# Performance work log

Measured on AMD Instinct MI355X. Metric: run time of the kernel, lower is better.

## Reference

```python
import jax, jax.numpy as jnp
import numpy as np

N_NODES = 100000
N_EDGES = 1600000
D_IN = 256
D_OUT = 64
BN_EPS = 1e-5


def setup_inputs() -> dict:
    key = jax.random.key(0)
    ks = jax.random.split(key, 8)
    x = jax.random.normal(ks[0], (N_NODES, D_IN), dtype=jnp.float32)
    edge_index = jax.random.randint(ks[1], (2, N_EDGES), 0, N_NODES, dtype=jnp.int32)
    W = jax.random.normal(ks[2], (D_OUT, D_IN), dtype=jnp.float32) / np.sqrt(D_IN).astype(np.float32)
    bias = 0.01 * jax.random.normal(ks[3], (D_OUT,), dtype=jnp.float32)
    gamma = 1.0 + 0.1 * jax.random.normal(ks[4], (D_OUT,), dtype=jnp.float32)
    beta = 0.1 * jax.random.normal(ks[5], (D_OUT,), dtype=jnp.float32)
    running_mean = 0.1 * jax.random.normal(ks[6], (D_OUT,), dtype=jnp.float32)
    running_var = jax.random.uniform(ks[7], (D_OUT,), dtype=jnp.float32, minval=0.5, maxval=1.5)
    return {"x": x, "edge_index": edge_index, "W": W, "bias": bias,
            "gamma": gamma, "beta": beta,
            "running_mean": running_mean, "running_var": running_var}


def reference(x, edge_index, W, bias, gamma, beta, running_mean, running_var):
    # GCNConv (PyG semantics): transform -> symmetric-normalized scatter-add with
    # self-loops (edge_weight = ones, self-loop weight = 1), then +bias.
    n = x.shape[0]
    loop = jnp.arange(n, dtype=edge_index.dtype)
    row = jnp.concatenate([edge_index[0], loop])  # source nodes
    col = jnp.concatenate([edge_index[1], loop])  # target nodes
    w = jnp.ones(row.shape[0], dtype=x.dtype)
    deg = jax.ops.segment_sum(w, col, num_segments=n)          # [N]
    dinv = jnp.where(deg > 0, jax.lax.rsqrt(deg), 0.0)          # D^{-1/2}
    norm = dinv[row] * w * dinv[col]                            # [E+N]
    xw = x @ W.T                                                # [N, D_OUT]
    agg = jax.ops.segment_sum(norm[:, None] * xw[row], col, num_segments=n)
    out = agg + bias
    # BatchNorm1d in eval mode (running stats); dropout inactive in eval.
    out = (out - running_mean) * jax.lax.rsqrt(running_var + BN_EPS) * gamma + beta
    return jax.nn.relu(out)
```

## Files before the change

### kernel.cpp

```cpp
#include <hip/hip_runtime.h>
#include <hip/hip_bf16.h>

#define D_IN 256
#define D_OUT 64
#define BN_EPS 1e-5f

#define BINSHIFT 8
#define BINCAP 4608
#define PCHUNK 8192

typedef __attribute__((ext_vector_type(4))) float floatx4;
typedef __attribute__((ext_vector_type(8))) __bf16 bf16x8;
typedef __attribute__((ext_vector_type(4))) unsigned uintx4;

__global__ __launch_bounds__(256) void k_prep(
        const float* __restrict__ W, __bf16* __restrict__ whi, __bf16* __restrict__ wlo,
        const float* __restrict__ bias, const float* __restrict__ gamma,
        const float* __restrict__ beta, const float* __restrict__ rmean,
        const float* __restrict__ rvar,
        float* __restrict__ bnsc, float* __restrict__ bnsh,
        int* __restrict__ bincur, int nbins) {
    int b = blockIdx.x, t = threadIdx.x;
    if (b < 2) {
        int i = b * 256 + t;
        if (i < nbins) bincur[i] = 0;
        if (b == 1 && t < D_OUT) {
            float sc = rsqrtf(rvar[t] + BN_EPS) * gamma[t];
            bnsc[t] = sc;
            bnsh[t] = (bias[t] - rmean[t]) * sc + beta[t];
        }
        return;
    }
    int tid = (b - 2) * 256 + t;
    int lane = tid & 63, c = (tid >> 6) & 7, tt = tid >> 9;
    int row = tt * 16 + (lane & 15);
    int k0 = c * 32 + (lane >> 4) * 8;
    size_t dst = (size_t)tid * 8;
    #pragma unroll
    for (int j = 0; j < 8; ++j) {
        float w = W[(size_t)row * D_IN + k0 + j];
        __bf16 h = (__bf16)w;
        whi[dst + j] = h;
        wlo[dst + j] = (__bf16)(w - (float)h);
    }
}

__global__ __launch_bounds__(256) void k_part(
        const int* __restrict__ ei, int* __restrict__ bincur,
        unsigned* __restrict__ pairs, int E, int nbins) {
    __shared__ int hist[512];
    __shared__ int base[512];
    int t = threadIdx.x;
    int e0 = blockIdx.x * PCHUNK;

    for (int j = t; j < nbins; j += 256) hist[j] = 0;
    __syncthreads();

    int cols[PCHUNK / 256];
    int ranks[PCHUNK / 256];
    #pragma unroll
    for (int i = 0; i < PCHUNK / 256; ++i) {
        int e = e0 + i * 256 + t;
        if (e < E) {
            int c = ei[E + e];
            cols[i] = c;
            ranks[i] = atomicAdd(&hist[c >> BINSHIFT], 1);
        }
    }
    __syncthreads();
    for (int j = t; j < nbins; j += 256)
        base[j] = atomicAdd(&bincur[j], hist[j]);
    __syncthreads();
    #pragma unroll
    for (int i = 0; i < PCHUNK / 256; ++i) {
        int e = e0 + i * 256 + t;
        if (e < E) {
            int c = cols[i];
            int bin = c >> BINSHIFT;
            int pos = base[bin] + ranks[i];
            if (pos >= BINCAP) pos = BINCAP - 1;
            pairs[(size_t)bin * BINCAP + pos] =
                ((unsigned)ei[e] << 8) | (unsigned)(c & 255);
        }
    }
}

__global__ __launch_bounds__(256) void k_binscan(
        const int* __restrict__ bincur, int* __restrict__ binoff,
        int* __restrict__ off, int nbins, int N) {
    __shared__ int sc[256];
    int t = threadIdx.x;
    int i0 = 2 * t, i1 = 2 * t + 1;
    int v0 = (i0 < nbins) ? bincur[i0] : 0;
    int v1 = (i1 < nbins) ? bincur[i1] : 0;
    int s = v0 + v1;
    sc[t] = s;
    __syncthreads();
    for (int o = 1; o < 256; o <<= 1) {
        int v = (t >= o) ? sc[t - o] : 0;
        __syncthreads();
        sc[t] += v;
        __syncthreads();
    }
    int excl = sc[t] - s;
    if (i0 < nbins) binoff[i0] = excl;
    if (i1 < nbins) binoff[i1] = excl + v0;
    if (t == 255) off[N] = sc[255];
}

__global__ __launch_bounds__(256) void k_fill3(
        const unsigned* __restrict__ pairs, const int* __restrict__ bincur,
        const int* __restrict__ binoff, int* __restrict__ off,
        float* __restrict__ dinv, int* __restrict__ srcs, int n) {
    __shared__ int hist[256];
    __shared__ int sc[256];
    __shared__ int curs[256];
    int bin = blockIdx.x, t = threadIdx.x;
    hist[t] = 0;
    __syncthreads();
    int cnt = bincur[bin];
    const unsigned* bp = pairs + (size_t)bin * BINCAP;
    for (int p = t; p < cnt; p += 256)
        atomicAdd(&hist[bp[p] & 255u], 1);
    __syncthreads();
    int own = hist[t];
    sc[t] = own;
    __syncthreads();
    for (int o = 1; o < 256; o <<= 1) {
        int v = (t >= o) ? sc[t - o] : 0;
        __syncthreads();
        sc[t] += v;
        __syncthreads();
    }
    int base = binoff[bin] + sc[t] - own;
    int node = (bin << BINSHIFT) + t;
    curs[t] = base;
    if (node < n) {
        off[node] = base;
        dinv[node] = rsqrtf((float)(own + 1));
    }
    __syncthreads();
    for (int p = t; p < cnt; p += 256) {
        unsigned v = bp[p];
        int pos = atomicAdd(&curs[v & 255u], 1);
        srcs[pos] = (int)(v >> 8);
    }
}

__global__ __launch_bounds__(256) void k_gemm(
        const float* __restrict__ x, const __bf16* __restrict__ whi,
        const __bf16* __restrict__ wlo, const float* __restrict__ dinv,
        __bf16* __restrict__ yb, int n) {
    int wave = threadIdx.x >> 6;
    int lane = threadIdx.x & 63;
    int m0 = blockIdx.x * 64 + wave * 16;
    if (m0 >= n) return;
    int q = lane >> 4, cl = lane & 15;
    int arow = m0 + cl; if (arow >= n) arow = n - 1;
    const float* ap = x + (size_t)arow * D_IN + q * 8;

    floatx4 acc[4] = {{0.f,0.f,0.f,0.f},{0.f,0.f,0.f,0.f},
                      {0.f,0.f,0.f,0.f},{0.f,0.f,0.f,0.f}};

    #pragma unroll
    for (int c = 0; c < 8; ++c) {
        floatx4 a0 = *(const floatx4*)(ap + c * 32);
        floatx4 a1 = *(const floatx4*)(ap + c * 32 + 4);
        bf16x8 ahi, alo;
        #pragma unroll
        for (int j = 0; j < 4; ++j) {
            __bf16 h0 = (__bf16)a0[j];
            __bf16 h1 = (__bf16)a1[j];
            ahi[j] = h0;     alo[j] = (__bf16)(a0[j] - (float)h0);
            ahi[4 + j] = h1; alo[4 + j] = (__bf16)(a1[j] - (float)h1);
        }
        #pragma unroll
        for (int t = 0; t < 4; ++t) {
            size_t fo = ((size_t)(t * 8 + c) * 64 + lane) * 8;
            bf16x8 bh = *(const bf16x8*)(whi + fo);
            bf16x8 bl = *(const bf16x8*)(wlo + fo);
            acc[t] = __builtin_amdgcn_mfma_f32_16x16x32_bf16(ahi, bh, acc[t], 0, 0, 0);
            acc[t] = __builtin_amdgcn_mfma_f32_16x16x32_bf16(alo, bh, acc[t], 0, 0, 0);
            acc[t] = __builtin_amdgcn_mfma_f32_16x16x32_bf16(ahi, bl, acc[t], 0, 0, 0);
        }
    }

    int nb = m0 + q * 4;
    float dv[4];
    #pragma unroll
    for (int r = 0; r < 4; ++r) dv[r] = (nb + r < n) ? dinv[nb + r] : 0.f;
    #pragma unroll
    for (int t = 0; t < 4; ++t) {
        #pragma unroll
        for (int r = 0; r < 4; ++r) {
            int node = nb + r;
            if (node < n)
                yb[(size_t)node * D_OUT + t * 16 + cl] = (__bf16)(dv[r] * acc[t][r]);
        }
    }
}

__device__ __forceinline__ void acc_row4(uintx4 v, float (&a)[8]) {
    #pragma unroll
    for (int k = 0; k < 4; ++k) {
        a[2 * k]     += __uint_as_float(v[k] << 16);
        a[2 * k + 1] += __uint_as_float(v[k] & 0xffff0000u);
    }
}

__global__ __launch_bounds__(256) void k_aggregate(
        const int* __restrict__ off, const int* __restrict__ srcs,
        const unsigned* __restrict__ ybf, const float* __restrict__ dinv,
        const float* __restrict__ bnsc, const float* __restrict__ bnsh,
        float* __restrict__ out, int n) {
    int node = blockIdx.x * 4 + (threadIdx.x >> 6);
    if (node >= n) return;
    int lane = threadIdx.x & 63;
    int g = lane >> 3, sl = lane & 7;
    int s = off[node], e2 = off[node + 1];

    float a[8] = {0.f, 0.f, 0.f, 0.f, 0.f, 0.f, 0.f, 0.f};
    float dv = 0.f;
    floatx4 bs0, bs1, bh0, bh1;
    if (g == 0) {
        dv = dinv[node];
        bs0 = *(const floatx4*)(bnsc + sl * 8);
        bs1 = *(const floatx4*)(bnsc + sl * 8 + 4);
        bh0 = *(const floatx4*)(bnsh + sl * 8);
        bh1 = *(const floatx4*)(bnsh + sl * 8 + 4);
        uintx4 v = *(const uintx4*)(ybf + (size_t)node * 32 + sl * 4);
        acc_row4(v, a);
    }

    int e = s + g;
    for (; e + 24 < e2; e += 32) {
        int r0 = srcs[e], r1 = srcs[e + 8], r2 = srcs[e + 16], r3 = srcs[e + 24];
        uintx4 v0 = *(const uintx4*)(ybf + (size_t)r0 * 32 + sl * 4);
        uintx4 v1 = *(const uintx4*)(ybf + (size_t)r1 * 32 + sl * 4);
        uintx4 v2 = *(const uintx4*)(ybf + (size_t)r2 * 32 + sl * 4);
        uintx4 v3 = *(const uintx4*)(ybf + (size_t)r3 * 32 + sl * 4);
        acc_row4(v0, a);
        acc_row4(v1, a);
        acc_row4(v2, a);
        acc_row4(v3, a);
    }
    for (; e + 8 < e2; e += 16) {
        int r0 = srcs[e], r1 = srcs[e + 8];
        uintx4 v0 = *(const uintx4*)(ybf + (size_t)r0 * 32 + sl * 4);
        uintx4 v1 = *(const uintx4*)(ybf + (size_t)r1 * 32 + sl * 4);
        acc_row4(v0, a);
        acc_row4(v1, a);
    }
    for (; e < e2; e += 8) {
        uintx4 v = *(const uintx4*)(ybf + (size_t)srcs[e] * 32 + sl * 4);
        acc_row4(v, a);
    }

    #pragma unroll
    for (int k = 0; k < 8; ++k) {
        a[k] += __shfl_xor(a[k], 8);
        a[k] += __shfl_xor(a[k], 16);
        a[k] += __shfl_xor(a[k], 32);
    }

    if (g == 0) {
        float o[8];
        #pragma unroll
        for (int k = 0; k < 4; ++k) {
            o[k]     = fmaf(dv * a[k],     bs0[k], bh0[k]);
            o[4 + k] = fmaf(dv * a[4 + k], bs1[k], bh1[k]);
        }
        floatx4 w0 = { fmaxf(o[0], 0.f), fmaxf(o[1], 0.f),
                       fmaxf(o[2], 0.f), fmaxf(o[3], 0.f) };
        floatx4 w1 = { fmaxf(o[4], 0.f), fmaxf(o[5], 0.f),
                       fmaxf(o[6], 0.f), fmaxf(o[7], 0.f) };
        *(floatx4*)(out + (size_t)node * D_OUT + sl * 8) = w0;
        *(floatx4*)(out + (size_t)node * D_OUT + sl * 8 + 4) = w1;
    }
}

static inline char* align_up(char* p, size_t a) {
    return (char*)(((uintptr_t)p + a - 1) & ~(uintptr_t)(a - 1));
}

extern "C" void kernel_launch(void* const* d_in, const int* in_sizes, int n_in,
                              void* d_out, int out_size, void* d_ws, size_t ws_size,
                              hipStream_t stream) {
    const float* x     = (const float*)d_in[0];
    const int*   ei    = (const int*)d_in[1];
    const float* W     = (const float*)d_in[2];
    const float* bias  = (const float*)d_in[3];
    const float* gamma = (const float*)d_in[4];
    const float* beta  = (const float*)d_in[5];
    const float* rmean = (const float*)d_in[6];
    const float* rvar  = (const float*)d_in[7];
    float* out = (float*)d_out;

    int N = in_sizes[0] / D_IN;
    int E = in_sizes[1] / 2;
    int nbins = (N + (1 << BINSHIFT) - 1) >> BINSHIFT;

    char* p = (char*)d_ws;
    int*      bincur = (int*)p;         p += 512 * 4;
    int*      binoff = (int*)p;         p += 512 * 4;
    int*      off    = (int*)p;         p += (size_t)(N + 1) * 4; p = align_up(p, 256);
    float*    dinv   = (float*)p;       p += (size_t)N * 4;       p = align_up(p, 256);
    float*    bnsc   = (float*)p;       p += D_OUT * 4;
    float*    bnsh   = (float*)p;       p += D_OUT * 4;           p = align_up(p, 256);
    __bf16*   whi    = (__bf16*)p;      p += (size_t)D_OUT * D_IN * 2; p = align_up(p, 256);
    __bf16*   wlo    = (__bf16*)p;      p += (size_t)D_OUT * D_IN * 2; p = align_up(p, 256);
    __bf16*   yb     = (__bf16*)p;      p += (size_t)N * D_OUT * 2;    p = align_up(p, 256);
    int*      srcs   = (int*)p;         p += (size_t)E * 4;       p = align_up(p, 256);
    unsigned* pairs  = (unsigned*)p;

    k_prep<<<10, 256, 0, stream>>>(W, whi, wlo, bias, gamma, beta, rmean, rvar,
                                   bnsc, bnsh, bincur, nbins);
    k_part<<<(E + PCHUNK - 1) / PCHUNK, 256, 0, stream>>>(ei, bincur, pairs, E, nbins);
    k_binscan<<<1, 256, 0, stream>>>(bincur, binoff, off, nbins, N);
    k_fill3<<<nbins, 256, 0, stream>>>(pairs, bincur, binoff, off, dinv, srcs, N);
    k_gemm<<<(N + 63) / 64, 256, 0, stream>>>(x, whi, wlo, dinv, yb, N);
    k_aggregate<<<(N + 3) / 4, 256, 0, stream>>>(off, srcs, (const unsigned*)yb,
                                                 dinv, bnsc, bnsh, out, N);
}
```

Measured before the change: 289.2 us.

## Fuse partition, bin scan and fill into one cooperative kernel with grid sync

Merges the three CSR-build kernels (edge partition into bins, bin prefix scan, per-bin fill) into a single cooperative launch with nbins blocks separated by grid-wide syncs. Each block now partitions about E/nbins edges instead of a fixed 8192-edge chunk. Edges beyond the first 16 per thread fall back to global atomics on the bin counters. This removes two kernel launches and their gaps, but the partition phase now runs on 391 blocks instead of 196, and the fallback path makes more global atomics.

```diff
diff --git a/kernel.cpp b/kernel.cpp
--- a/kernel.cpp
+++ b/kernel.cpp
@@ -1,5 +1,8 @@
 #include <hip/hip_runtime.h>
 #include <hip/hip_bf16.h>
+#include <hip/hip_cooperative_groups.h>
+
+namespace cg = cooperative_groups;
 
 #define D_IN 256
 #define D_OUT 64
@@ -7,7 +10,6 @@
 
 #define BINSHIFT 8
 #define BINCAP 4608
-#define PCHUNK 8192
 
 typedef __attribute__((ext_vector_type(4))) float floatx4;
 typedef __attribute__((ext_vector_type(8))) __bf16 bf16x8;
@@ -45,23 +47,31 @@
     }
 }
 
-__global__ __launch_bounds__(256) void k_part(
+__global__ __launch_bounds__(256) void k_build(
         const int* __restrict__ ei, int* __restrict__ bincur,
-        unsigned* __restrict__ pairs, int E, int nbins) {
+        unsigned* __restrict__ pairs, int* __restrict__ binoff,
+        int* __restrict__ off, float* __restrict__ dinv,
+        int* __restrict__ srcs, int E, int N, int nbins) {
     __shared__ int hist[512];
     __shared__ int base[512];
-    int t = threadIdx.x;
-    int e0 = blockIdx.x * PCHUNK;
+    __shared__ int curs[256];
+    int t = threadIdx.x, b = blockIdx.x;
+    cg::grid_group grid = cg::this_grid();
+
+    int nb = gridDim.x;
+    int chunk = (E + nb - 1) / nb;
+    int e0 = b * chunk;
+    int eend = e0 + chunk; if (eend > E) eend = E;
 
     for (int j = t; j < nbins; j += 256) hist[j] = 0;
     __syncthreads();
 
-    int cols[PCHUNK / 256];
-    int ranks[PCHUNK / 256];
-    #pragma unroll
-    for (int i = 0; i < PCHUNK / 256; ++i) {
+    int cols[16];
+    int ranks[16];
+    #pragma unroll
+    for (int i = 0; i < 16; ++i) {
         int e = e0 + i * 256 + t;
-        if (e < E) {
+        if (e < eend) {
             int c = ei[E + e];
             cols[i] = c;
             ranks[i] = atomicAdd(&hist[c >> BINSHIFT], 1);
@@ -72,9 +82,9 @@
         base[j] = atomicAdd(&bincur[j], hist[j]);
     __syncthreads();
     #pragma unroll
-    for (int i = 0; i < PCHUNK / 256; ++i) {
+    for (int i = 0; i < 16; ++i) {
         int e = e0 + i * 256 + t;
-        if (e < E) {
+        if (e < eend) {
             int c = cols[i];
             int bin = c >> BINSHIFT;
             int pos = base[bin] + ranks[i];
@@ -83,60 +93,59 @@
                 ((unsigned)ei[e] << 8) | (unsigned)(c & 255);
         }
     }
-}
-
-__global__ __launch_bounds__(256) void k_binscan(
-        const int* __restrict__ bincur, int* __restrict__ binoff,
-        int* __restrict__ off, int nbins, int N) {
-    __shared__ int sc[256];
-    int t = threadIdx.x;
-    int i0 = 2 * t, i1 = 2 * t + 1;
-    int v0 = (i0 < nbins) ? bincur[i0] : 0;
-    int v1 = (i1 < nbins) ? bincur[i1] : 0;
-    int s = v0 + v1;
-    sc[t] = s;
-    __syncthreads();
-    for (int o = 1; o < 256; o <<= 1) {
-        int v = (t >= o) ? sc[t - o] : 0;
+    for (int e = e0 + 16 * 256 + t; e < eend; e += 256) {
+        int c = ei[E + e];
+        int bin = c >> BINSHIFT;
+        int pos = atomicAdd(&bincur[bin], 1);
+        if (pos >= BINCAP) pos = BINCAP - 1;
+        pairs[(size_t)bin * BINCAP + pos] =
+            ((unsigned)ei[e] << 8) | (unsigned)(c & 255);
+    }
+
+    grid.sync();
+
+    if (b == 0) {
+        int i0 = 2 * t, i1 = 2 * t + 1;
+        int v0 = (i0 < nbins) ? bincur[i0] : 0;
+        int v1 = (i1 < nbins) ? bincur[i1] : 0;
+        int s = v0 + v1;
+        base[t] = s;
         __syncthreads();
-        sc[t] += v;
-        __syncthreads();
-    }
-    int excl = sc[t] - s;
-    if (i0 < nbins) binoff[i0] = excl;
-    if (i1 < nbins) binoff[i1] = excl + v0;
-    if (t == 255) off[N] = sc[255];
-}
-
-__global__ __launch_bounds__(256) void k_fill3(
-        const unsigned* __restrict__ pairs, const int* __restrict__ bincur,
-        const int* __restrict__ binoff, int* __restrict__ off,
-        float* __restrict__ dinv, int* __restrict__ srcs, int n) {
-    __shared__ int hist[256];
-    __shared__ int sc[256];
-    __shared__ int curs[256];
-    int bin = blockIdx.x, t = threadIdx.x;
+        for (int o = 1; o < 256; o <<= 1) {
+            int v = (t >= o) ? base[t - o] : 0;
+            __syncthreads();
+            base[t] += v;
+            __syncthreads();
+        }
+        int excl = base[t] - s;
+        if (i0 < nbins) binoff[i0] = excl;
+        if (i1 < nbins) binoff[i1] = excl + v0;
+        if (t == 255) off[N] = base[255];
+    }
+
+    grid.sync();
+
     hist[t] = 0;
     __syncthreads();
-    int cnt = bincur[bin];
-    const unsigned* bp = pairs + (size_t)bin * BINCAP;
+    int cnt = bincur[b];
+    const unsigned* bp = pairs + (size_t)b * BINCAP;
     for (int p = t; p < cnt; p += 256)
         atomicAdd(&hist[bp[p] & 255u], 1);
     __syncthreads();
     int own = hist[t];
-    sc[t] = own;
+    base[t] = own;
     __syncthreads();
     for (int o = 1; o < 256; o <<= 1) {
-        int v = (t >= o) ? sc[t - o] : 0;
+        int v = (t >= o) ? base[t - o] : 0;
         __syncthreads();
-        sc[t] += v;
+        base[t] += v;
         __syncthreads();
     }
-    int base = binoff[bin] + sc[t] - own;
-    int node = (bin << BINSHIFT) + t;
-    curs[t] = base;
-    if (node < n) {
-        off[node] = base;
+    int nbase = binoff[b] + base[t] - own;
+    int node = (b << BINSHIFT) + t;
+    curs[t] = nbase;
+    if (node < N) {
+        off[node] = nbase;
         dinv[node] = rsqrtf((float)(own + 1));
     }
     __syncthreads();
@@ -315,9 +324,15 @@
 
     k_prep<<<10, 256, 0, stream>>>(W, whi, wlo, bias, gamma, beta, rmean, rvar,
                                    bnsc, bnsh, bincur, nbins);
-    k_part<<<(E + PCHUNK - 1) / PCHUNK, 256, 0, stream>>>(ei, bincur, pairs, E, nbins);
-    k_binscan<<<1, 256, 0, stream>>>(bincur, binoff, off, nbins, N);
-    k_fill3<<<nbins, 256, 0, stream>>>(pairs, bincur, binoff, off, dinv, srcs, N);
+
+    {
+        void* args[] = { (void*)&ei, (void*)&bincur, (void*)&pairs,
+                         (void*)&binoff, (void*)&off, (void*)&dinv,
+                         (void*)&srcs, (void*)&E, (void*)&N, (void*)&nbins };
+        hipLaunchCooperativeKernel((void*)k_build, dim3(nbins), dim3(256),
+                                   args, 0, stream);
+    }
+
     k_gemm<<<(N + 63) / 64, 256, 0, stream>>>(x, whi, wlo, dinv, yb, N);
     k_aggregate<<<(N + 3) / 4, 256, 0, stream>>>(off, srcs, (const unsigned*)yb,
                                                  dinv, bnsc, bnsh, out, N);
```

New measurement: 405.1 us. +40.1%, slower.
